# Kernel optimization log

Measured on AMD Instinct MI355X. Metric: run time of the kernel, lower is better.

Reference implementation:

```python
import jax, jax.numpy as jnp
import numpy as np
from jax import lax

SCALE = 1.0
DENSE = 4
ITERS = 5


def setup_inputs() -> dict:
    key = jax.random.key(0)
    k1, k2, k3 = jax.random.split(key, 3)
    N, C, H, W = 32, 3, 512, 512
    A = 512
    data = jax.random.normal(k1, (N, C, H, W), dtype=jnp.float32)
    attx = jax.random.uniform(k2, (N, A), dtype=jnp.float32)
    atty = jax.random.uniform(k3, (N, A), dtype=jnp.float32)
    return {"data": data, "attx": attx, "atty": atty}


def _water_fill(attx, atty, out_size, out_sizey, in_size):
    # iterative water-filling clamp: 5 sequential max/min/sum/update passes
    att_size = attx.shape[1]
    att_sizey = atty.shape[1]
    thr0 = (SCALE * DENSE * in_size) / att_size
    ax = attx * out_size
    ay = atty * out_sizey
    for j in range(ITERS):
        mx = jnp.max(ax, axis=1, keepdims=True)
        my = jnp.max(ay, axis=1, keepdims=True)
        thr = jnp.minimum(mx, my)
        if j == 0:
            thr = jnp.minimum(thr, thr0)
        ax = jnp.minimum(ax, thr)
        ay = jnp.minimum(ay, thr)
        ax = ax + (out_size - jnp.sum(ax, axis=1, keepdims=True)) / att_size
        ay = ay + (out_sizey - jnp.sum(ay, axis=1, keepdims=True)) / att_sizey
    # as in the source: first element forced to 1 before cumsum
    ax = ax.at[:, 0].set(1.0)
    ay = ay.at[:, 0].set(1.0)
    return jnp.cumsum(ax, axis=1), jnp.cumsum(ay, axis=1), ax, ay


def _coords(att, cs, out_n):
    # inverse-CDF mapping: for each of out_n uniform steps of the sampled axis,
    # find the source bin in cumsum cs and interpolate -> coord in [-1,1]
    A = att.shape[1]
    step = cs[:, -1] / out_n                                   # (N,)
    t = jnp.arange(1, out_n + 1, dtype=cs.dtype)[None, :] * step[:, None]  # (N,out_n)

    def per_sample(cs_n, att_n, t_n):
        j = jnp.clip(jnp.searchsorted(cs_n, t_n, side='left'), 0, A - 1)
        prev = jnp.where(j > 0, cs_n[jnp.maximum(j - 1, 0)], 0.0)
        frac = (t_n - prev) / jnp.maximum(att_n[j], 1e-12)
        return (j.astype(cs_n.dtype) + frac) / A * 2.0 - 1.0

    return jax.vmap(per_sample)(cs, att, t)


def _grid_sample(data, grid):
    # F.grid_sample, bilinear, padding_mode='zeros', align_corners=False
    N, C, H, W = data.shape
    x = (grid[..., 0] + 1.0) * (W / 2.0) - 0.5   # (N,Ho,Wo)
    y = (grid[..., 1] + 1.0) * (H / 2.0) - 0.5
    x0 = jnp.floor(x)
    y0 = jnp.floor(y)
    x1 = x0 + 1.0
    y1 = y0 + 1.0
    wx1 = x - x0
    wx0 = 1.0 - wx1
    wy1 = y - y0
    wy0 = 1.0 - wy1

    def gather(ix, iy):
        valid = (ix >= 0) & (ix < W) & (iy >= 0) & (iy < H)
        ixc = jnp.clip(ix, 0, W - 1).astype(jnp.int32)
        iyc = jnp.clip(iy, 0, H - 1).astype(jnp.int32)
        v = jax.vmap(lambda d, iy_n, ix_n: d[:, iy_n, ix_n])(data, iyc, ixc)  # (N,C,Ho,Wo)
        return v * valid[:, None, :, :].astype(data.dtype)

    out = (gather(x0, y0) * (wx0 * wy0)[:, None]
           + gather(x1, y0) * (wx1 * wy0)[:, None]
           + gather(x0, y1) * (wx0 * wy1)[:, None]
           + gather(x1, y1) * (wx1 * wy1)[:, None])
    return out


def reference(data, attx, atty):
    N, C, H, W = data.shape
    out_size = int(H * SCALE)
    out_sizey = int(W * SCALE)
    # grid is built from detached attention (data.detach()/att.detach() in source)
    ax_ = lax.stop_gradient(attx)
    ay_ = lax.stop_gradient(atty)
    csx, csy, ax, ay = _water_fill(ax_, ay_, out_size, out_sizey, H)
    gy = _coords(ax, csx, out_size)    # height coords, (N,out_size)
    gx = _coords(ay, csy, out_sizey)   # width coords,  (N,out_sizey)
    grid = jnp.stack([
        jnp.broadcast_to(gx[:, None, :], (N, out_size, out_sizey)),
        jnp.broadcast_to(gy[:, :, None], (N, out_size, out_sizey)),
    ], axis=-1)  # (N,Ho,Wo,2)
    grid = lax.stop_gradient(grid)
    sampled = _grid_sample(data, grid)
    return sampled, grid
```

## Files before the change

kernel.cpp:

```cpp
#include <hip/hip_runtime.h>
#include <hip/hip_bf16.h>

#define AN 512
#define NB 32
#define HW 512

__global__ __launch_bounds__(512) void waterfill_coords_kernel(
    const float* __restrict__ attx, const float* __restrict__ atty,
    float* __restrict__ gx, float* __restrict__ gy)
{
    __shared__ float axs[AN], ays[AN], csx[AN], csy[AN], redx[AN], redy[AN];
    const int n = blockIdx.x;
    const int t = threadIdx.x;

    float ax = attx[n * AN + t] * 512.0f;
    float ay = atty[n * AN + t] * 512.0f;

    for (int j = 0; j < 5; ++j) {
        redx[t] = ax; redy[t] = ay;
        __syncthreads();
        for (int s = 256; s > 0; s >>= 1) {
            if (t < s) {
                redx[t] = fmaxf(redx[t], redx[t + s]);
                redy[t] = fmaxf(redy[t], redy[t + s]);
            }
            __syncthreads();
        }
        float thr = fminf(redx[0], redy[0]);
        if (j == 0) thr = fminf(thr, 4.0f);
        __syncthreads();

        ax = fminf(ax, thr);
        ay = fminf(ay, thr);

        redx[t] = ax; redy[t] = ay;
        __syncthreads();
        for (int s = 256; s > 0; s >>= 1) {
            if (t < s) {
                redx[t] = redx[t] + redx[t + s];
                redy[t] = redy[t] + redy[t + s];
            }
            __syncthreads();
        }
        float corx = (512.0f - redx[0]) / 512.0f;
        float cory = (512.0f - redy[0]) / 512.0f;
        __syncthreads();
        ax += corx;
        ay += cory;
    }

    if (t == 0) { ax = 1.0f; ay = 1.0f; }
    axs[t] = ax; ays[t] = ay;
    __syncthreads();

    if (t == 0) {
        float run = 0.0f;
        for (int i = 0; i < AN; ++i) { run += axs[i]; csx[i] = run; }
    }
    if (t == 64) {
        float run = 0.0f;
        for (int i = 0; i < AN; ++i) { run += ays[i]; csy[i] = run; }
    }
    __syncthreads();

    {
        float step = csx[AN - 1] / 512.0f;
        float tv = (float)(t + 1) * step;
        int lo = 0, hi = AN;
        while (lo < hi) {
            int mid = (lo + hi) >> 1;
            if (csx[mid] < tv) lo = mid + 1; else hi = mid;
        }
        int j = lo > (AN - 1) ? (AN - 1) : lo;
        float prev = (j > 0) ? csx[j - 1] : 0.0f;
        float frac = (tv - prev) / fmaxf(axs[j], 1e-12f);
        gy[n * AN + t] = ((float)j + frac) / 512.0f * 2.0f - 1.0f;
    }
    {
        float step = csy[AN - 1] / 512.0f;
        float tv = (float)(t + 1) * step;
        int lo = 0, hi = AN;
        while (lo < hi) {
            int mid = (lo + hi) >> 1;
            if (csy[mid] < tv) lo = mid + 1; else hi = mid;
        }
        int j = lo > (AN - 1) ? (AN - 1) : lo;
        float prev = (j > 0) ? csy[j - 1] : 0.0f;
        float frac = (tv - prev) / fmaxf(ays[j], 1e-12f);
        gx[n * AN + t] = ((float)j + frac) / 512.0f * 2.0f - 1.0f;
    }
}

__global__ __launch_bounds__(256) void grid_sample_kernel(
    const float* __restrict__ data, const float* __restrict__ gx,
    const float* __restrict__ gy, float* __restrict__ outS,
    float* __restrict__ outG)
{
    const int wo = blockIdx.x * 256 + threadIdx.x;
    const int ho = blockIdx.y;
    const int n  = blockIdx.z;

    const float gxv = gx[n * AN + wo];
    const float gyv = gy[n * AN + ho];

    float2 g2; g2.x = gxv; g2.y = gyv;
    ((float2*)outG)[((size_t)n * HW + ho) * HW + wo] = g2;

    const float x = (gxv + 1.0f) * 256.0f - 0.5f;
    const float y = (gyv + 1.0f) * 256.0f - 0.5f;
    const float x0f = floorf(x), y0f = floorf(y);
    const float x1f = x0f + 1.0f, y1f = y0f + 1.0f;
    const float wx1 = x - x0f, wx0 = 1.0f - wx1;
    const float wy1 = y - y0f, wy0 = 1.0f - wy1;

    const bool vx0 = (x0f >= 0.0f) && (x0f < 512.0f);
    const bool vx1 = (x1f >= 0.0f) && (x1f < 512.0f);
    const bool vy0 = (y0f >= 0.0f) && (y0f < 512.0f);
    const bool vy1 = (y1f >= 0.0f) && (y1f < 512.0f);

    const int x0 = (int)fminf(fmaxf(x0f, 0.0f), 511.0f);
    const int x1 = (int)fminf(fmaxf(x1f, 0.0f), 511.0f);
    const int y0 = (int)fminf(fmaxf(y0f, 0.0f), 511.0f);
    const int y1 = (int)fminf(fmaxf(y1f, 0.0f), 511.0f);

    const float w00 = wx0 * wy0, w10 = wx1 * wy0;
    const float w01 = wx0 * wy1, w11 = wx1 * wy1;

    const float* base = data + (size_t)n * 3 * HW * HW;
    const size_t r0 = (size_t)y0 * HW, r1 = (size_t)y1 * HW;
    size_t o = (((size_t)n * 3) * HW + ho) * HW + wo;

    #pragma unroll
    for (int c = 0; c < 3; ++c) {
        const float* p = base + (size_t)c * HW * HW;
        const float v00 = (vx0 && vy0) ? p[r0 + x0] : 0.0f;
        const float v10 = (vx1 && vy0) ? p[r0 + x1] : 0.0f;
        const float v01 = (vx0 && vy1) ? p[r1 + x0] : 0.0f;
        const float v11 = (vx1 && vy1) ? p[r1 + x1] : 0.0f;
        outS[o + (size_t)c * HW * HW] = v00 * w00 + v10 * w10 + v01 * w01 + v11 * w11;
    }
}

extern "C" void kernel_launch(void* const* d_in, const int* in_sizes, int n_in,
                              void* d_out, int out_size, void* d_ws, size_t ws_size,
                              hipStream_t stream) {
    const float* data = (const float*)d_in[0];
    const float* attx = (const float*)d_in[1];
    const float* atty = (const float*)d_in[2];

    float* gx = (float*)d_ws;
    float* gy = gx + NB * AN;

    float* outS = (float*)d_out;
    float* outG = outS + (size_t)NB * 3 * HW * HW;

    waterfill_coords_kernel<<<NB, AN, 0, stream>>>(attx, atty, gx, gy);

    dim3 grid(HW / 256, HW, NB);
    grid_sample_kernel<<<grid, 256, 0, stream>>>(data, gx, gy, outS, outG);
}
```

Baseline: 269.6 us.

## Vectorize grid-sample to 4 outputs per thread and use wave-shuffle reductions

Measured after the change: 295.1 us. 1.09x slower.

```diff
diff --git a/kernel.cpp b/kernel.cpp
--- a/kernel.cpp
+++ b/kernel.cpp
@@ -5,89 +5,86 @@
 #define NB 32
 #define HW 512
 
+__device__ __forceinline__ float waveMax(float v) {
+    #pragma unroll
+    for (int off = 32; off > 0; off >>= 1) v = fmaxf(v, __shfl_xor(v, off, 64));
+    return v;
+}
+__device__ __forceinline__ float waveSum(float v) {
+    #pragma unroll
+    for (int off = 32; off > 0; off >>= 1) v += __shfl_xor(v, off, 64);
+    return v;
+}
+
 __global__ __launch_bounds__(512) void waterfill_coords_kernel(
     const float* __restrict__ attx, const float* __restrict__ atty,
     float* __restrict__ gx, float* __restrict__ gy)
 {
-    __shared__ float axs[AN], ays[AN], csx[AN], csy[AN], redx[AN], redy[AN];
+    __shared__ float axs[AN], ays[AN], csx[AN], csy[AN];
+    __shared__ float wrx[8], wry[8];
     const int n = blockIdx.x;
     const int t = threadIdx.x;
+    const int wid = t >> 6;
 
     float ax = attx[n * AN + t] * 512.0f;
     float ay = atty[n * AN + t] * 512.0f;
 
     for (int j = 0; j < 5; ++j) {
-        redx[t] = ax; redy[t] = ay;
+        float mx = waveMax(ax), my = waveMax(ay);
+        if ((t & 63) == 0) { wrx[wid] = mx; wry[wid] = my; }
         __syncthreads();
-        for (int s = 256; s > 0; s >>= 1) {
-            if (t < s) {
-                redx[t] = fmaxf(redx[t], redx[t + s]);
-                redy[t] = fmaxf(redy[t], redy[t + s]);
-            }
-            __syncthreads();
-        }
-        float thr = fminf(redx[0], redy[0]);
+        float Mx = wrx[0], My = wry[0];
+        #pragma unroll
+        for (int i = 1; i < 8; ++i) { Mx = fmaxf(Mx, wrx[i]); My = fmaxf(My, wry[i]); }
+        float thr = fminf(Mx, My);
         if (j == 0) thr = fminf(thr, 4.0f);
-        __syncthreads();
-
         ax = fminf(ax, thr);
         ay = fminf(ay, thr);
 
-        redx[t] = ax; redy[t] = ay;
+        float sx = waveSum(ax), sy = waveSum(ay);
         __syncthreads();
-        for (int s = 256; s > 0; s >>= 1) {
-            if (t < s) {
-                redx[t] = redx[t] + redx[t + s];
-                redy[t] = redy[t] + redy[t + s];
-            }
-            __syncthreads();
-        }
-        float corx = (512.0f - redx[0]) / 512.0f;
-        float cory = (512.0f - redy[0]) / 512.0f;
+        if ((t & 63) == 0) { wrx[wid] = sx; wry[wid] = sy; }
         __syncthreads();
-        ax += corx;
-        ay += cory;
+        float Sx = 0.0f, Sy = 0.0f;
+        #pragma unroll
+        for (int i = 0; i < 8; ++i) { Sx += wrx[i]; Sy += wry[i]; }
+        ax += (512.0f - Sx) / 512.0f;
+        ay += (512.0f - Sy) / 512.0f;
+        __syncthreads();
     }
 
     if (t == 0) { ax = 1.0f; ay = 1.0f; }
-    axs[t] = ax; ays[t] = ay;
+    axs[t] = ax; ays[t] = ay; csx[t] = ax; csy[t] = ay;
     __syncthreads();
 
-    if (t == 0) {
-        float run = 0.0f;
-        for (int i = 0; i < AN; ++i) { run += axs[i]; csx[i] = run; }
+    #pragma unroll
+    for (int s = 1; s < AN; s <<= 1) {
+        float vx = (t >= s) ? csx[t - s] : 0.0f;
+        float vy = (t >= s) ? csy[t - s] : 0.0f;
+        __syncthreads();
+        csx[t] += vx; csy[t] += vy;
+        __syncthreads();
     }
-    if (t == 64) {
-        float run = 0.0f;
-        for (int i = 0; i < AN; ++i) { run += ays[i]; csy[i] = run; }
-    }
-    __syncthreads();
 
     {
         float step = csx[AN - 1] / 512.0f;
         float tv = (float)(t + 1) * step;
         int lo = 0, hi = AN;
-        while (lo < hi) {
-            int mid = (lo + hi) >> 1;
-            if (csx[mid] < tv) lo = mid + 1; else hi = mid;
-        }
+        while (lo < hi) { int mid = (lo + hi) >> 1; if (csx[mid] < tv) lo = mid + 1; else hi = mid; }
         int j = lo > (AN - 1) ? (AN - 1) : lo;
         float prev = (j > 0) ? csx[j - 1] : 0.0f;
         float frac = (tv - prev) / fmaxf(axs[j], 1e-12f);
-        gy[n * AN + t] = ((float)j + frac) / 512.0f * 2.0f - 1.0f;
+        gy[n * AN + t] = ((float)j + frac) * (2.0f / 512.0f) - 1.0f;
     }
     {
         float step = csy[AN - 1] / 512.0f;
         float tv = (float)(t + 1) * step;
         int lo = 0, hi = AN;
-        while (lo < hi) {
-            int mid = (lo + hi) >> 1;
-            if (csy[mid] < tv) lo = mid + 1; else hi = mid;
-        }
+        while (lo < hi) { int mid = (lo + hi) >> 1; if (csy[mid] < tv) lo = mid + 1; else hi = mid; }
         int j = lo > (AN - 1) ? (AN - 1) : lo;
         float prev = (j > 0) ? csy[j - 1] : 0.0f;
         float frac = (tv - prev) / fmaxf(ays[j], 1e-12f);
-        gx[n * AN + t] = ((float)j + frac) / 512.0f * 2.0f - 1.0f;
+        gx[n * AN + t] = ((float)j + frac) * (2.0f / 512.0f) - 1.0f;
     }
 }
 
@@ -96,49 +93,61 @@
     const float* __restrict__ gy, float* __restrict__ outS,
     float* __restrict__ outG)
 {
-    const int wo = blockIdx.x * 256 + threadIdx.x;
-    const int ho = blockIdx.y;
-    const int n  = blockIdx.z;
+    const int lane   = threadIdx.x & 127;
+    const int rowsel = threadIdx.x >> 7;
+    const int ho = blockIdx.x * 2 + rowsel;
+    const int n  = blockIdx.y;
+    const int wo = lane * 4;
 
-    const float gxv = gx[n * AN + wo];
     const float gyv = gy[n * AN + ho];
+    const float4 gx4 = ((const float4*)(gx + n * AN))[lane];
 
-    float2 g2; g2.x = gxv; g2.y = gyv;
-    ((float2*)outG)[((size_t)n * HW + ho) * HW + wo] = g2;
-
-    const float x = (gxv + 1.0f) * 256.0f - 0.5f;
-    const float y = (gyv + 1.0f) * 256.0f - 0.5f;
-    const float x0f = floorf(x), y0f = floorf(y);
-    const float x1f = x0f + 1.0f, y1f = y0f + 1.0f;
-    const float wx1 = x - x0f, wx0 = 1.0f - wx1;
+    const float y   = (gyv + 1.0f) * 256.0f - 0.5f;
+    const float y0f = floorf(y);
     const float wy1 = y - y0f, wy0 = 1.0f - wy1;
-
-    const bool vx0 = (x0f >= 0.0f) && (x0f < 512.0f);
-    const bool vx1 = (x1f >= 0.0f) && (x1f < 512.0f);
-    const bool vy0 = (y0f >= 0.0f) && (y0f < 512.0f);
-    const bool vy1 = (y1f >= 0.0f) && (y1f < 512.0f);
-
-    const int x0 = (int)fminf(fmaxf(x0f, 0.0f), 511.0f);
-    const int x1 = (int)fminf(fmaxf(x1f, 0.0f), 511.0f);
+    const float vy0 = ((y0f >= 0.0f) & (y0f < 512.0f)) ? 1.0f : 0.0f;
+    const float vy1 = ((y0f >= -1.0f) & (y0f < 511.0f)) ? 1.0f : 0.0f;
     const int y0 = (int)fminf(fmaxf(y0f, 0.0f), 511.0f);
-    const int y1 = (int)fminf(fmaxf(y1f, 0.0f), 511.0f);
-
-    const float w00 = wx0 * wy0, w10 = wx1 * wy0;
-    const float w01 = wx0 * wy1, w11 = wx1 * wy1;
+    const int y1 = (int)fminf(fmaxf(y0f + 1.0f, 0.0f), 511.0f);
+    const size_t r0 = (size_t)y0 * HW, r1 = (size_t)y1 * HW;
 
     const float* base = data + (size_t)n * 3 * HW * HW;
-    const size_t r0 = (size_t)y0 * HW, r1 = (size_t)y1 * HW;
-    size_t o = (((size_t)n * 3) * HW + ho) * HW + wo;
+    float res[3][4];
+    float gv[8];
+    const float xg[4] = {gx4.x, gx4.y, gx4.z, gx4.w};
 
     #pragma unroll
-    for (int c = 0; c < 3; ++c) {
-        const float* p = base + (size_t)c * HW * HW;
-        const float v00 = (vx0 && vy0) ? p[r0 + x0] : 0.0f;
-        const float v10 = (vx1 && vy0) ? p[r0 + x1] : 0.0f;
-        const float v01 = (vx0 && vy1) ? p[r1 + x0] : 0.0f;
-        const float v11 = (vx1 && vy1) ? p[r1 + x1] : 0.0f;
-        outS[o + (size_t)c * HW * HW] = v00 * w00 + v10 * w10 + v01 * w01 + v11 * w11;
+    for (int k = 0; k < 4; ++k) {
+        const float gxv = xg[k];
+        gv[2 * k] = gxv; gv[2 * k + 1] = gyv;
+        const float x   = (gxv + 1.0f) * 256.0f - 0.5f;
+        const float x0f = floorf(x);
+        const float wx1 = x - x0f, wx0 = 1.0f - wx1;
+        const float vx0 = ((x0f >= 0.0f) & (x0f < 512.0f)) ? 1.0f : 0.0f;
+        const float vx1 = ((x0f >= -1.0f) & (x0f < 511.0f)) ? 1.0f : 0.0f;
+        const int x0 = (int)fminf(fmaxf(x0f, 0.0f), 511.0f);
+        const int x1 = (int)fminf(fmaxf(x0f + 1.0f, 0.0f), 511.0f);
+        const float w00 = wx0 * wy0 * vx0 * vy0;
+        const float w10 = wx1 * wy0 * vx1 * vy0;
+        const float w01 = wx0 * wy1 * vx0 * vy1;
+        const float w11 = wx1 * wy1 * vx1 * vy1;
+        #pragma unroll
+        for (int c = 0; c < 3; ++c) {
+            const float* p = base + (size_t)c * HW * HW;
+            res[c][k] = p[r0 + x0] * w00 + p[r0 + x1] * w10
+                      + p[r1 + x0] * w01 + p[r1 + x1] * w11;
+        }
     }
+
+    const size_t o = (((size_t)n * 3) * HW + ho) * HW + wo;
+    #pragma unroll
+    for (int c = 0; c < 3; ++c)
+        *(float4*)(outS + o + (size_t)c * HW * HW) =
+            make_float4(res[c][0], res[c][1], res[c][2], res[c][3]);
+
+    float4* gptr = (float4*)(outG + (((size_t)n * HW + ho) * HW + wo) * 2);
+    gptr[0] = make_float4(gv[0], gv[1], gv[2], gv[3]);
+    gptr[1] = make_float4(gv[4], gv[5], gv[6], gv[7]);
 }
 
 extern "C" void kernel_launch(void* const* d_in, const int* in_sizes, int n_in,
@@ -156,6 +165,6 @@
 
     waterfill_coords_kernel<<<NB, AN, 0, stream>>>(attx, atty, gx, gy);
 
-    dim3 grid(HW / 256, HW, NB);
+    dim3 grid(HW / 2, NB);
     grid_sample_kernel<<<grid, 256, 0, stream>>>(data, gx, gy, outS, outG);
 }
```
